# Optimization experiments

Hardware: AMD Instinct MI355X
Metric: run time of the kernel (lower is better)

## Reference

```python
import jax, jax.numpy as jnp
import numpy as np

E = 2048
H = 16
DH = E // H  # 128
B, T = 2, 2048
EPS = 1e-8


def rmsnorm(x, g):
    rms = jnp.sqrt(jnp.mean(x * x, axis=-1, keepdims=True) + EPS)
    return g * (x / rms)


def setup_inputs() -> dict:
    key = jax.random.key(0)
    ks = jax.random.split(key, 16)
    s_in = 1.0 / np.sqrt(E)
    s_ff = 1.0 / np.sqrt(4 * E)
    return {
        "x": jax.random.normal(ks[0], (B, T, E), dtype=jnp.float32),
        # stacked per-head QKV projections, stored (in, out) so y = x @ W + b
        "wq": jax.random.normal(ks[1], (H, E, DH), dtype=jnp.float32) * s_in,
        "bq": jax.random.normal(ks[2], (H, DH), dtype=jnp.float32) * s_in,
        "wk": jax.random.normal(ks[3], (H, E, DH), dtype=jnp.float32) * s_in,
        "bk": jax.random.normal(ks[4], (H, DH), dtype=jnp.float32) * s_in,
        "wv": jax.random.normal(ks[5], (H, E, DH), dtype=jnp.float32) * s_in,
        "bv": jax.random.normal(ks[6], (H, DH), dtype=jnp.float32) * s_in,
        "wo": jax.random.normal(ks[7], (E, E), dtype=jnp.float32) * s_in,
        "bo": jax.random.normal(ks[8], (E,), dtype=jnp.float32) * s_in,
        "w1": jax.random.normal(ks[9], (E, 4 * E), dtype=jnp.float32) * s_in,
        "b1": jax.random.normal(ks[10], (4 * E,), dtype=jnp.float32) * s_in,
        "w2": jax.random.normal(ks[11], (4 * E, E), dtype=jnp.float32) * s_ff,
        "b2": jax.random.normal(ks[12], (E,), dtype=jnp.float32) * s_ff,
        "g1": jnp.ones((E,), dtype=jnp.float32),
        "g2": jnp.ones((E,), dtype=jnp.float32),
    }


def reference(x, wq, bq, wk, bk, wv, bv, wo, bo, w1, b1, w2, b2, g1, g2):
    b, t, e = x.shape
    # --- attention sublayer ---
    h = rmsnorm(x, g1)
    q = jnp.einsum("bte,hed->bhtd", h, wq) + bq[None, :, None, :]
    k = jnp.einsum("bte,hed->bhtd", h, wk) + bk[None, :, None, :]
    v = jnp.einsum("bte,hed->bhtd", h, wv) + bv[None, :, None, :]
    scores = jnp.einsum("bhtd,bhsd->bhts", q, k) / jnp.sqrt(jnp.float32(DH))
    causal = jnp.tril(jnp.ones((t, t), dtype=bool))
    scores = jnp.where(causal[None, None], scores, -jnp.inf)
    w = jax.nn.softmax(scores, axis=-1)
    o = jnp.einsum("bhts,bhsd->bhtd", w, v)
    o = o.transpose(0, 2, 1, 3).reshape(b, t, e)  # concat heads on last dim
    x = x + o @ wo + bo
    # --- FFN sublayer (exact GELU, dropout is identity at inference) ---
    h = rmsnorm(x, g2)
    x = x + jax.nn.gelu(h @ w1 + b1, approximate=False) @ w2 + b2
    return x
```

## Files before the change

### kernel.cpp

```cpp
#include <hip/hip_runtime.h>
#include <hip/hip_bf16.h>

typedef unsigned short u16;
typedef unsigned int   u32;
typedef __attribute__((ext_vector_type(8))) short short8;
typedef __attribute__((ext_vector_type(4))) float f32x4;
typedef __attribute__((ext_vector_type(4))) unsigned short u16x4;

#define E_    2048
#define H_    16
#define DH_   128
#define B_    2
#define T_    2048
#define NTOK  4096
#define QKVN  6144

#define VMCNT(n) asm volatile("s_waitcnt vmcnt(" #n ")" ::: "memory")
#define LGKM0()  asm volatile("s_waitcnt lgkmcnt(0)" ::: "memory")

__device__ __forceinline__ u16 f2bf(float f) {
  union { float f; u32 u; } v; v.f = f;
  u32 r = (v.u + 0x7FFFu + ((v.u >> 16) & 1u)) >> 16;
  return (u16)r;
}

__global__ __launch_bounds__(256) void tr64(
    const float* __restrict__ in, u16* __restrict__ out,
    int R, int C, size_t inZ, size_t outZ)
{
  __shared__ float t[64][65];
  const float* ib = in + (size_t)blockIdx.z * inZ;
  u16* ob = out + (size_t)blockIdx.z * outZ;
  const int r0 = blockIdx.y * 64, c0 = blockIdx.x * 64;
  const int tid = threadIdx.x;
  const int rr = tid >> 4;
  const int cc = (tid & 15) * 4;
  #pragma unroll
  for (int p = 0; p < 4; ++p) {
    const float4 v = *(const float4*)(ib + (size_t)(r0 + p * 16 + rr) * C + c0 + cc);
    t[cc + 0][p * 16 + rr] = v.x;
    t[cc + 1][p * 16 + rr] = v.y;
    t[cc + 2][p * 16 + rr] = v.z;
    t[cc + 3][p * 16 + rr] = v.w;
  }
  __syncthreads();
  const int wr = tid >> 3;
  const int wc = (tid & 7) * 8;
  #pragma unroll
  for (int p = 0; p < 2; ++p) {
    short8 s;
    #pragma unroll
    for (int j = 0; j < 8; ++j) s[j] = (short)f2bf(t[p * 32 + wr][wc + j]);
    *(short8*)(ob + (size_t)(c0 + p * 32 + wr) * R + r0 + wc) = s;
  }
}

__global__ __launch_bounds__(256) void bias_cat(
    const float* __restrict__ bq, const float* __restrict__ bk,
    const float* __restrict__ bv, float* __restrict__ bias)
{
  int idx = blockIdx.x * 256 + threadIdx.x;
  const float* bb = (idx < 2048) ? bq : (idx < 4096) ? bk : bv;
  bias[idx] = bb[idx & 2047];
}

__global__ __launch_bounds__(256) void rmsnorm_k(
    const float* __restrict__ x, const float* __restrict__ g, u16* __restrict__ o)
{
  const int row = blockIdx.x;
  const float4* xr = (const float4*)(x + (size_t)row * E_);
  const float4* gr = (const float4*)g;
  const int tid = threadIdx.x;
  float4 a0 = xr[tid], a1 = xr[tid + 256];
  float s = a0.x*a0.x + a0.y*a0.y + a0.z*a0.z + a0.w*a0.w
          + a1.x*a1.x + a1.y*a1.y + a1.z*a1.z + a1.w*a1.w;
  #pragma unroll
  for (int m = 1; m < 64; m <<= 1) s += __shfl_xor(s, m);
  __shared__ float wsum[4];
  if ((tid & 63) == 0) wsum[tid >> 6] = s;
  __syncthreads();
  float tot = wsum[0] + wsum[1] + wsum[2] + wsum[3];
  float rinv = rsqrtf(tot * (1.0f / E_) + 1e-8f);
  float4 g0 = gr[tid], g1 = gr[tid + 256];
  u16x4 o0, o1;
  o0[0] = f2bf(a0.x * g0.x * rinv); o0[1] = f2bf(a0.y * g0.y * rinv);
  o0[2] = f2bf(a0.z * g0.z * rinv); o0[3] = f2bf(a0.w * g0.w * rinv);
  o1[0] = f2bf(a1.x * g1.x * rinv); o1[1] = f2bf(a1.y * g1.y * rinv);
  o1[2] = f2bf(a1.z * g1.z * rinv); o1[3] = f2bf(a1.w * g1.w * rinv);
  u16x4* orow = (u16x4*)(o + (size_t)row * E_);
  orow[tid] = o0;
  orow[tid + 256] = o1;
}

__device__ __forceinline__ void gload_lds16(const void* g, u16* lds_base) {
  __builtin_amdgcn_global_load_lds(
      (const __attribute__((address_space(1))) u32*)g,
      (__attribute__((address_space(3))) u32*)lds_base, 16, 0, 0);
}

template<int BM, int BN, int EPI>
__global__ __launch_bounds__(512, 2)
void gemm3(const u16* __restrict__ A, const u16* __restrict__ Bt,
           const float* __restrict__ bias, const float* __restrict__ resid,
           void* __restrict__ out, int M, int N, int K)
{
  constexpr int WROWS = BM / 2;
  constexpr int WCOLS = BN / 4;
  constexpr int MR    = WROWS / 16;
  constexpr int BUF   = (BM + BN) * 32;
  __shared__ __align__(16) u16 sh[3 * BUF];

  const int tid  = threadIdx.x;
  const int lane = tid & 63;
  const int l15  = lane & 15, lg = lane >> 4;
  const int w    = tid >> 6;
  const int wm   = w >> 2;
  const int wn   = w & 3;
  const int xs   = (l15 >> 1) & 3;

  const int nbx = N / BN;
  const int nwg = nbx * (M / BM);
  const int q8  = nwg >> 3;
  const int sid = (blockIdx.x & 7) * q8 + (blockIdx.x >> 3);
  const int m0  = (sid / nbx) * BM;
  const int n0  = (sid % nbx) * BN;

  const int r0 = tid >> 2;
  const int c0 = (((tid & 3) ^ ((tid >> 3) & 3)) * 8);
  const u16* gA  = A  + (size_t)(m0 + r0) * K + c0;
  const u16* gB  = Bt + (size_t)(n0 + r0) * K + c0;
  const u16* gA2 = gA + (size_t)128 * K;
  const u16* gB2 = gB + (size_t)128 * K;
  const int wub = (tid & ~63) * 8;

  f32x4 acc[MR][4] = {};
  const int NT = K >> 5;

  #pragma unroll
  for (int t = 0; t < 2; ++t) {
    u16* wb = sh + t * BUF;
    const int kS = t * 32;
    if constexpr (BM == 256) {
      gload_lds16(gA  + kS, wb + wub);
      gload_lds16(gA2 + kS, wb + 512 * 8 + wub);
      gload_lds16(gB  + kS, wb + 1024 * 8 + wub);
      gload_lds16(gB2 + kS, wb + 1536 * 8 + wub);
    } else {
      gload_lds16(gA  + kS, wb + wub);
      gload_lds16(gB  + kS, wb + 512 * 8 + wub);
      gload_lds16(gB2 + kS, wb + 1024 * 8 + wub);
    }
  }
  if constexpr (BM == 256) VMCNT(4); else VMCNT(3);
  __builtin_amdgcn_s_barrier();
  __builtin_amdgcn_sched_barrier(0);

  int b0 = 0, b2 = 2;
  #pragma unroll 1
  for (int i = 0; i < NT; ++i) {
    const u16* rb = sh + b0 * BUF;
    u16* wb = sh + b2 * BUF;
    const bool st = (i + 2 < NT);
    const int kS = (i + 2) << 5;
    short8 af[4], bf[4];

    if constexpr (BM == 256) {
      #pragma unroll
      for (int n = 0; n < 4; ++n)
        bf[n] = *(const short8*)(rb + BM * 32 + (wn * WCOLS + n * 16 + l15) * 32 + ((lg ^ xs) * 8));
      #pragma unroll
      for (int m = 0; m < 4; ++m)
        af[m] = *(const short8*)(rb + (wm * WROWS + m * 16 + l15) * 32 + ((lg ^ xs) * 8));
      if (st) {
        gload_lds16(gA + kS, wb + wub);
        gload_lds16(gB + kS, wb + 1024 * 8 + wub);
      }
      __builtin_amdgcn_s_barrier();
      LGKM0();
      __builtin_amdgcn_sched_barrier(0);
      __builtin_amdgcn_s_setprio(1);
      #pragma unroll
      for (int m = 0; m < 4; ++m)
        #pragma unroll
        for (int n = 0; n < 4; ++n)
          acc[m][n] = __builtin_amdgcn_mfma_f32_16x16x32_bf16(af[m], bf[n], acc[m][n], 0, 0, 0);
      __builtin_amdgcn_s_setprio(0);
      __builtin_amdgcn_s_barrier();
      __builtin_amdgcn_sched_barrier(0);
      #pragma unroll
      for (int m = 0; m < 4; ++m)
        af[m] = *(const short8*)(rb + (wm * WROWS + (4 + m) * 16 + l15) * 32 + ((lg ^ xs) * 8));
      if (st) {
        gload_lds16(gA2 + kS, wb + 512 * 8 + wub);
        gload_lds16(gB2 + kS, wb + 1536 * 8 + wub);
      }
      __builtin_amdgcn_s_barrier();
      LGKM0();
      __builtin_amdgcn_sched_barrier(0);
      __builtin_amdgcn_s_setprio(1);
      #pragma unroll
      for (int m = 0; m < 4; ++m)
        #pragma unroll
        for (int n = 0; n < 4; ++n)
          acc[4 + m][n] = __builtin_amdgcn_mfma_f32_16x16x32_bf16(af[m], bf[n], acc[4 + m][n], 0, 0, 0);
      __builtin_amdgcn_s_setprio(0);
      VMCNT(4);
      __builtin_amdgcn_s_barrier();
      __builtin_amdgcn_sched_barrier(0);
    } else {
      #pragma unroll
      for (int n = 0; n < 4; ++n)
        bf[n] = *(const short8*)(rb + BM * 32 + (wn * WCOLS + n * 16 + l15) * 32 + ((lg ^ xs) * 8));
      #pragma unroll
      for (int m = 0; m < 4; ++m)
        af[m] = *(const short8*)(rb + (wm * WROWS + m * 16 + l15) * 32 + ((lg ^ xs) * 8));
      if (st) {
        gload_lds16(gA  + kS, wb + wub);
        gload_lds16(gB  + kS, wb + 512 * 8 + wub);
        gload_lds16(gB2 + kS, wb + 1024 * 8 + wub);
      }
      __builtin_amdgcn_s_barrier();
      LGKM0();
      __builtin_amdgcn_sched_barrier(0);
      __builtin_amdgcn_s_setprio(1);
      #pragma unroll
      for (int m = 0; m < 4; ++m)
        #pragma unroll
        for (int n = 0; n < 4; ++n)
          acc[m][n] = __builtin_amdgcn_mfma_f32_16x16x32_bf16(af[m], bf[n], acc[m][n], 0, 0, 0);
      __builtin_amdgcn_s_setprio(0);
      VMCNT(3);
      __builtin_amdgcn_s_barrier();
      __builtin_amdgcn_sched_barrier(0);
    }
    b0 = (b0 == 2) ? 0 : b0 + 1;
    b2 = (b2 == 2) ? 0 : b2 + 1;
  }

  float bv[4];
  #pragma unroll
  for (int n = 0; n < 4; ++n) bv[n] = bias[n0 + wn * WCOLS + n * 16 + l15];

  if constexpr (EPI == 1) {
    #pragma unroll
    for (int n = 0; n < 4; ++n) {
      const int col = n0 + wn * WCOLS + n * 16 + l15;
      #pragma unroll
      for (int m = 0; m < MR; ++m)
        #pragma unroll
        for (int r = 0; r < 4; ++r) {
          const int row = m0 + wm * WROWS + m * 16 + lg * 4 + r;
          const size_t off = (size_t)row * N + col;
          ((float*)out)[off] = acc[m][n][r] + bv[n] + resid[off];
        }
    }
  } else {
    u16* ep = sh + w * 1024;
    #pragma unroll
    for (int m = 0; m < MR; ++m) {
      LGKM0();
      __builtin_amdgcn_sched_barrier(0);
      #pragma unroll
      for (int n = 0; n < 4; ++n)
        #pragma unroll
        for (int r = 0; r < 4; ++r) {
          float v = acc[m][n][r] + bv[n];
          if (EPI == 2) v = 0.5f * v * (1.0f + erff(v * 0.70710678118654752f));
          ep[(lg * 4 + r) * 64 + n * 16 + l15] = f2bf(v);
        }
      LGKM0();
      __builtin_amdgcn_sched_barrier(0);
      const int row0 = m0 + wm * WROWS + m * 16;
      #pragma unroll
      for (int it = 0; it < 2; ++it) {
        const int ch = it * 64 + lane;
        const int rr = ch >> 3, c8 = ch & 7;
        short8 s = *(const short8*)(ep + rr * 64 + c8 * 8);
        *(short8*)((u16*)out + (size_t)(row0 + rr) * N + n0 + wn * WCOLS + c8 * 8) = s;
      }
    }
  }
}

__global__ __launch_bounds__(256) void vtrans_k(
    const u16* __restrict__ qkv, u16* __restrict__ vt)
{
  __shared__ u16 tile[DH_][66];
  const int tid = threadIdx.x;
  const int bid = blockIdx.x;
  const int tt = bid & 31;
  const int bh = bid >> 5;
  const int b  = bh >> 4, h = bh & 15;
  const int t0 = tt * 64;
  const u16* src = qkv + (size_t)b * T_ * QKVN + 2 * E_ + h * DH_;
  #pragma unroll
  for (int it = 0; it < 8; ++it) {
    int c = it * 256 + tid;
    int t = c >> 5, dc = c & 31;
    u16x4 v = *(const u16x4*)(src + (size_t)(t0 + t) * QKVN + dc * 4);
    #pragma unroll
    for (int j = 0; j < 4; ++j) tile[dc * 4 + j][t] = v[j];
  }
  __syncthreads();
  u16* dst = vt + (size_t)bh * DH_ * T_ + t0;
  #pragma unroll
  for (int it = 0; it < 8; ++it) {
    int c = it * 256 + tid;
    int d = c >> 4, tc = c & 15;
    u16x4 v;
    #pragma unroll
    for (int j = 0; j < 4; ++j) v[j] = tile[d][tc * 4 + j];
    *(u16x4*)(dst + (size_t)d * T_ + tc * 4) = v;
  }
}

__global__ __launch_bounds__(256) void attn_k(
    const u16* __restrict__ qkv, const u16* __restrict__ vt, u16* __restrict__ o)
{
  const int tid  = threadIdx.x;
  const int lane = tid & 63;
  const int w    = tid >> 6;
  const int l15  = lane & 15, lg = lane >> 4;
  const int bid  = blockIdx.x;
  const int pair = bid & 31;
  const int qt   = 15 - (bid >> 5);
  const int h    = pair & 15;
  const int b    = pair >> 4;
  const int Q0 = qt * 128;
  const int qw = Q0 + w * 32;

  __shared__ __align__(16) u16 Ks[2][64 * 128];
  __shared__ __align__(16) u16 Vs[2][128 * 64];
  __shared__ __align__(16) u16 Ps[4][32 * 64];

  const u16* qb  = qkv + (size_t)b * T_ * QKVN + h * DH_;
  const u16* kb  = qb + E_;
  const u16* vtb = vt + (size_t)(b * H_ + h) * DH_ * T_;

  short8 qf[2][4];
  #pragma unroll
  for (int qi = 0; qi < 2; ++qi)
    #pragma unroll
    for (int kk = 0; kk < 4; ++kk)
      qf[qi][kk] = *(const short8*)(qb + (size_t)(qw + qi * 16 + l15) * QKVN + kk * 32 + lg * 8);

  f32x4 oacc[2][8] = {};
  float m_[2][4], l_[2][4];
  #pragma unroll
  for (int qi = 0; qi < 2; ++qi)
    #pragma unroll
    for (int r = 0; r < 4; ++r) { m_[qi][r] = -1e30f; l_[qi][r] = 0.f; }

  const int xr = l15 & 7;
  const float scl = 0.08838834764831845f;
  const int nt = Q0 / 64 + 2;
  const int qmaxw = qw + 31;
  const int wub = (tid & ~63);

  const u16* kp[4]; const u16* vp[4];
  #pragma unroll
  for (int i = 0; i < 4; ++i) {
    int f = i * 256 + tid;
    int r = f >> 4, p = f & 15, c = p ^ (r & 7);
    kp[i] = kb + (size_t)r * QKVN + c * 8;
  }
  #pragma unroll
  for (int i = 0; i < 4; ++i) {
    int f = i * 256 + tid;
    int d = f >> 3, p = f & 7, c = p ^ (d & 7);
    vp[i] = vtb + (size_t)d * T_ + c * 8;
  }

  auto STAGEKV = [&](int s0, int bufi) {
    const size_t ko = (size_t)s0 * QKVN;
    #pragma unroll
    for (int i = 0; i < 4; ++i)
      gload_lds16(kp[i] + ko, &Ks[bufi][(i * 256 + wub) * 8]);
    #pragma unroll
    for (int i = 0; i < 4; ++i)
      gload_lds16(vp[i] + s0, &Vs[bufi][(i * 256 + wub) * 8]);
  };

  STAGEKV(0, 0);
  VMCNT(0);
  __builtin_amdgcn_s_barrier();
  __builtin_amdgcn_sched_barrier(0);

  #pragma unroll 1
  for (int st = 0; st < nt; ++st) {
    const int s0 = st * 64;
    const int cur = st & 1;
    if (st + 1 < nt) STAGEKV(s0 + 64, cur ^ 1);

    if (s0 <= qmaxw) {
      const u16* Kc = Ks[cur];
      const u16* Vc = Vs[cur];
      f32x4 sc[2][4] = {};
      __builtin_amdgcn_s_setprio(1);
      #pragma unroll
      for (int sj = 0; sj < 4; ++sj) {
        const int row = sj * 16 + l15;
        #pragma unroll
        for (int kk = 0; kk < 4; ++kk) {
          short8 kfr = *(const short8*)(Kc + row * 128 + (((kk * 4 + lg) ^ xr) * 8));
          sc[0][sj] = __builtin_amdgcn_mfma_f32_16x16x32_bf16(qf[0][kk], kfr, sc[0][sj], 0, 0, 0);
          sc[1][sj] = __builtin_amdgcn_mfma_f32_16x16x32_bf16(qf[1][kk], kfr, sc[1][sj], 0, 0, 0);
        }
      }
      __builtin_amdgcn_s_setprio(0);
      const bool needmask = (s0 + 63 > qw);
      #pragma unroll
      for (int qi = 0; qi < 2; ++qi)
        #pragma unroll
        for (int sj = 0; sj < 4; ++sj)
          #pragma unroll
          for (int r = 0; r < 4; ++r) {
            float v = sc[qi][sj][r] * scl;
            if (needmask) {
              int s = s0 + sj * 16 + l15;
              int q = qw + qi * 16 + lg * 4 + r;
              if (s > q) v = -1e30f;
            }
            sc[qi][sj][r] = v;
          }
      #pragma unroll
      for (int qi = 0; qi < 2; ++qi) {
        float tmax[4], alpha[4], rsum[4];
        #pragma unroll
        for (int r = 0; r < 4; ++r)
          tmax[r] = fmaxf(fmaxf(sc[qi][0][r], sc[qi][1][r]), fmaxf(sc[qi][2][r], sc[qi][3][r]));
        #pragma unroll
        for (int r = 0; r < 4; ++r)
          #pragma unroll
          for (int m = 1; m < 16; m <<= 1) tmax[r] = fmaxf(tmax[r], __shfl_xor(tmax[r], m));
        #pragma unroll
        for (int r = 0; r < 4; ++r) {
          float mn = fmaxf(m_[qi][r], tmax[r]);
          alpha[r] = __expf(m_[qi][r] - mn);
          m_[qi][r] = mn;
          rsum[r] = 0.f;
        }
        #pragma unroll
        for (int sj = 0; sj < 4; ++sj)
          #pragma unroll
          for (int r = 0; r < 4; ++r) {
            float p = __expf(sc[qi][sj][r] - m_[qi][r]);
            rsum[r] += p;
            const int row = qi * 16 + lg * 4 + r;
            const int ch  = (sj * 2 + (l15 >> 3)) ^ (row & 7);
            Ps[w][row * 64 + ch * 8 + (l15 & 7)] = f2bf(p);
          }
        #pragma unroll
        for (int r = 0; r < 4; ++r) {
          #pragma unroll
          for (int m = 1; m < 16; m <<= 1) rsum[r] += __shfl_xor(rsum[r], m);
          l_[qi][r] = l_[qi][r] * alpha[r] + rsum[r];
        }
        #pragma unroll
        for (int dj = 0; dj < 8; ++dj)
          #pragma unroll
          for (int r = 0; r < 4; ++r) oacc[qi][dj][r] *= alpha[r];
      }
      LGKM0();
      __builtin_amdgcn_sched_barrier(0);
      __builtin_amdgcn_s_setprio(1);
      #pragma unroll
      for (int ks = 0; ks < 2; ++ks) {
        short8 pf0 = *(const short8*)(&Ps[w][l15 * 64 + (((ks * 4 + lg) ^ xr) * 8)]);
        short8 pf1 = *(const short8*)(&Ps[w][(16 + l15) * 64 + (((ks * 4 + lg) ^ xr) * 8)]);
        #pragma unroll
        for (int dj = 0; dj < 8; ++dj) {
          const int row = dj * 16 + l15;
          short8 vfr = *(const short8*)(Vc + row * 64 + (((ks * 4 + lg) ^ xr) * 8));
          oacc[0][dj] = __builtin_amdgcn_mfma_f32_16x16x32_bf16(pf0, vfr, oacc[0][dj], 0, 0, 0);
          oacc[1][dj] = __builtin_amdgcn_mfma_f32_16x16x32_bf16(pf1, vfr, oacc[1][dj], 0, 0, 0);
        }
      }
      __builtin_amdgcn_s_setprio(0);
    }
    VMCNT(0);
    __builtin_amdgcn_s_barrier();
    __builtin_amdgcn_sched_barrier(0);
  }

  float inv[2][4];
  #pragma unroll
  for (int qi = 0; qi < 2; ++qi)
    #pragma unroll
    for (int r = 0; r < 4; ++r) inv[qi][r] = 1.0f / l_[qi][r];
  u16* ob = o + (size_t)(b * T_ + qw) * E_ + h * DH_;
  #pragma unroll
  for (int qi = 0; qi < 2; ++qi)
    #pragma unroll
    for (int dj = 0; dj < 8; ++dj)
      #pragma unroll
      for (int r = 0; r < 4; ++r)
        ob[(size_t)(qi * 16 + lg * 4 + r) * E_ + dj * 16 + l15] = f2bf(oacc[qi][dj][r] * inv[qi][r]);
}

extern "C" void kernel_launch(void* const* d_in, const int* in_sizes, int n_in,
                              void* d_out, int out_size, void* d_ws, size_t ws_size,
                              hipStream_t stream)
{
  const float* x  = (const float*)d_in[0];
  const float* wq = (const float*)d_in[1];
  const float* bq = (const float*)d_in[2];
  const float* wk = (const float*)d_in[3];
  const float* bk = (const float*)d_in[4];
  const float* wv = (const float*)d_in[5];
  const float* bv = (const float*)d_in[6];
  const float* wo = (const float*)d_in[7];
  const float* bo = (const float*)d_in[8];
  const float* w1 = (const float*)d_in[9];
  const float* b1 = (const float*)d_in[10];
  const float* w2 = (const float*)d_in[11];
  const float* b2 = (const float*)d_in[12];
  const float* g1 = (const float*)d_in[13];
  const float* g2 = (const float*)d_in[14];
  float* xout = (float*)d_out;

  if (ws_size < 201351168u) return;

  char* ws = (char*)d_ws;
  u16*   wqkv_t = (u16*)(ws + 0);
  u16*   h1     = (u16*)(ws + 25165824);
  u16*   qkv    = (u16*)(ws + 41943040);
  u16*   vt     = (u16*)(ws + 92274688);
  u16*   o_     = (u16*)(ws + 109051904);
  u16*   wo_t   = (u16*)(ws + 125829120);
  u16*   w1_t   = (u16*)(ws + 134217728);
  u16*   w2_t   = (u16*)(ws + 167772160);
  float* bqkv   = (float*)(ws + 201326592);
  u16*   u_     = (u16*)(ws + 0);
  u16*   h2     = vt;
  float* x2     = xout;

  tr64<<<dim3(2, 32, 16), 256, 0, stream>>>(wq, wqkv_t,                          E_, DH_, (size_t)E_ * DH_, (size_t)DH_ * E_);
  tr64<<<dim3(2, 32, 16), 256, 0, stream>>>(wk, wqkv_t + (size_t)E_ * E_,        E_, DH_, (size_t)E_ * DH_, (size_t)DH_ * E_);
  tr64<<<dim3(2, 32, 16), 256, 0, stream>>>(wv, wqkv_t + (size_t)2 * E_ * E_,    E_, DH_, (size_t)E_ * DH_, (size_t)DH_ * E_);
  tr64<<<dim3(32, 32, 1),  256, 0, stream>>>(wo, wo_t, E_, E_, 0, 0);
  tr64<<<dim3(128, 32, 1), 256, 0, stream>>>(w1, w1_t, E_, 4 * E_, 0, 0);
  tr64<<<dim3(32, 128, 1), 256, 0, stream>>>(w2, w2_t, 4 * E_, E_, 0, 0);
  bias_cat<<<24, 256, 0, stream>>>(bq, bk, bv, bqkv);

  rmsnorm_k<<<NTOK, 256, 0, stream>>>(x, g1, h1);
  gemm3<128, 256, 0><<<(NTOK / 128) * (QKVN / 256), 512, 0, stream>>>(h1, wqkv_t, bqkv, nullptr, qkv, NTOK, QKVN, E_);
  vtrans_k<<<B_ * H_ * (T_ / 64), 256, 0, stream>>>(qkv, vt);
  attn_k<<<B_ * H_ * (T_ / 16 / 8), 256, 0, stream>>>(qkv, vt, o_);
  gemm3<128, 256, 1><<<(NTOK / 128) * (E_ / 256), 512, 0, stream>>>(o_, wo_t, bo, x, x2, NTOK, E_, E_);
  rmsnorm_k<<<NTOK, 256, 0, stream>>>(x2, g2, h2);
  gemm3<256, 256, 2><<<(NTOK / 256) * (4 * E_ / 256), 512, 0, stream>>>(h2, w1_t, b1, nullptr, u_, NTOK, 4 * E_, E_);
  gemm3<128, 256, 1><<<(NTOK / 128) * (E_ / 256), 512, 0, stream>>>(u_, w2_t, b2, x2, xout, NTOK, E_, 4 * E_);
}
```

Baseline: 728.3 us.

## Unroll GEMM K-loop by three buffers and drop manual lgkm waits and sched barriers

The GEMM main loop is unrolled three ways through a macro, so the triple-buffer indices become compile-time constants instead of rotating runtime variables. The tail drains vmcnt to zero on the last tiles. Explicit lgkmcnt(0) waits and sched_barrier fences are removed from the GEMM and attention loops, which lets the compiler interleave LDS reads with MFMAs. This gives up the hand-enforced instruction ordering, and it depends on the compiler inserting correct waits for LDS reads that are consumed after s_barrier, which is a correctness risk.

```diff
diff --git a/kernel.cpp b/kernel.cpp
--- a/kernel.cpp
+++ b/kernel.cpp
@@ -16,7 +16,6 @@
 #define QKVN  6144
 
 #define VMCNT(n) asm volatile("s_waitcnt vmcnt(" #n ")" ::: "memory")
-#define LGKM0()  asm volatile("s_waitcnt lgkmcnt(0)" ::: "memory")
 
 __device__ __forceinline__ u16 f2bf(float f) {
   union { float f; u32 u; } v; v.f = f;
@@ -153,89 +152,90 @@
   }
   if constexpr (BM == 256) VMCNT(4); else VMCNT(3);
   __builtin_amdgcn_s_barrier();
-  __builtin_amdgcn_sched_barrier(0);
-
-  int b0 = 0, b2 = 2;
+
+  int i = 0;
+
+#define KTILE(CUR, STG)                                                          \
+  do {                                                                           \
+    const u16* rb = sh + (CUR) * BUF;                                            \
+    u16* wb = sh + (STG) * BUF;                                                  \
+    const bool st = (i + 2 < NT);                                                \
+    const int kS = (i + 2) << 5;                                                 \
+    const int rem = NT - 1 - i;                                                  \
+    short8 af[4], bf[4];                                                         \
+    if constexpr (BM == 256) {                                                   \
+      _Pragma("unroll")                                                          \
+      for (int n = 0; n < 4; ++n)                                                \
+        bf[n] = *(const short8*)(rb + BM * 32 + (wn * WCOLS + n * 16 + l15) * 32 + ((lg ^ xs) * 8)); \
+      _Pragma("unroll")                                                          \
+      for (int m = 0; m < 4; ++m)                                                \
+        af[m] = *(const short8*)(rb + (wm * WROWS + m * 16 + l15) * 32 + ((lg ^ xs) * 8)); \
+      if (st) {                                                                  \
+        gload_lds16(gA + kS, wb + wub);                                          \
+        gload_lds16(gB + kS, wb + 1024 * 8 + wub);                               \
+      }                                                                          \
+      __builtin_amdgcn_s_barrier();                                              \
+      __builtin_amdgcn_s_setprio(1);                                             \
+      _Pragma("unroll")                                                          \
+      for (int m = 0; m < 4; ++m)                                                \
+        _Pragma("unroll")                                                        \
+        for (int n = 0; n < 4; ++n)                                              \
+          acc[m][n] = __builtin_amdgcn_mfma_f32_16x16x32_bf16(af[m], bf[n], acc[m][n], 0, 0, 0); \
+      __builtin_amdgcn_s_setprio(0);                                             \
+      __builtin_amdgcn_s_barrier();                                              \
+      _Pragma("unroll")                                                          \
+      for (int m = 0; m < 4; ++m)                                                \
+        af[m] = *(const short8*)(rb + (wm * WROWS + (4 + m) * 16 + l15) * 32 + ((lg ^ xs) * 8)); \
+      if (st) {                                                                  \
+        gload_lds16(gA2 + kS, wb + 512 * 8 + wub);                               \
+        gload_lds16(gB2 + kS, wb + 1536 * 8 + wub);                              \
+      }                                                                          \
+      __builtin_amdgcn_s_barrier();                                              \
+      __builtin_amdgcn_s_setprio(1);                                             \
+      _Pragma("unroll")                                                          \
+      for (int m = 0; m < 4; ++m)                                                \
+        _Pragma("unroll")                                                        \
+        for (int n = 0; n < 4; ++n)                                              \
+          acc[4 + m][n] = __builtin_amdgcn_mfma_f32_16x16x32_bf16(af[m], bf[n], acc[4 + m][n], 0, 0, 0); \
+      __builtin_amdgcn_s_setprio(0);                                             \
+      if (rem >= 2) { VMCNT(4); } else { VMCNT(0); }                             \
+      __builtin_amdgcn_s_barrier();                                              \
+    } else {                                                                     \
+      _Pragma("unroll")                                                          \
+      for (int n = 0; n < 4; ++n)                                                \
+        bf[n] = *(const short8*)(rb + BM * 32 + (wn * WCOLS + n * 16 + l15) * 32 + ((lg ^ xs) * 8)); \
+      _Pragma("unroll")                                                          \
+      for (int m = 0; m < 4; ++m)                                                \
+        af[m] = *(const short8*)(rb + (wm * WROWS + m * 16 + l15) * 32 + ((lg ^ xs) * 8)); \
+      if (st) {                                                                  \
+        gload_lds16(gA  + kS, wb + wub);                                         \
+        gload_lds16(gB  + kS, wb + 512 * 8 + wub);                               \
+        gload_lds16(gB2 + kS, wb + 1024 * 8 + wub);                              \
+      }                                                                          \
+      __builtin_amdgcn_s_barrier();                                              \
+      __builtin_amdgcn_s_setprio(1);                                             \
+      _Pragma("unroll")                                                          \
+      for (int m = 0; m < 4; ++m)                                                \
+        _Pragma("unroll")                                                        \
+        for (int n = 0; n < 4; ++n)                                              \
+          acc[m][n] = __builtin_amdgcn_mfma_f32_16x16x32_bf16(af[m], bf[n], acc[m][n], 0, 0, 0); \
+      __builtin_amdgcn_s_setprio(0);                                             \
+      if (rem >= 2) { VMCNT(3); } else { VMCNT(0); }                             \
+      __builtin_amdgcn_s_barrier();                                              \
+    }                                                                            \
+    ++i;                                                                         \
+  } while (0)
+
+  const int trips = NT / 3;
   #pragma unroll 1
-  for (int i = 0; i < NT; ++i) {
-    const u16* rb = sh + b0 * BUF;
-    u16* wb = sh + b2 * BUF;
-    const bool st = (i + 2 < NT);
-    const int kS = (i + 2) << 5;
-    short8 af[4], bf[4];
-
-    if constexpr (BM == 256) {
-      #pragma unroll
-      for (int n = 0; n < 4; ++n)
-        bf[n] = *(const short8*)(rb + BM * 32 + (wn * WCOLS + n * 16 + l15) * 32 + ((lg ^ xs) * 8));
-      #pragma unroll
-      for (int m = 0; m < 4; ++m)
-        af[m] = *(const short8*)(rb + (wm * WROWS + m * 16 + l15) * 32 + ((lg ^ xs) * 8));
-      if (st) {
-        gload_lds16(gA + kS, wb + wub);
-        gload_lds16(gB + kS, wb + 1024 * 8 + wub);
-      }
-      __builtin_amdgcn_s_barrier();
-      LGKM0();
-      __builtin_amdgcn_sched_barrier(0);
-      __builtin_amdgcn_s_setprio(1);
-      #pragma unroll
-      for (int m = 0; m < 4; ++m)
-        #pragma unroll
-        for (int n = 0; n < 4; ++n)
-          acc[m][n] = __builtin_amdgcn_mfma_f32_16x16x32_bf16(af[m], bf[n], acc[m][n], 0, 0, 0);
-      __builtin_amdgcn_s_setprio(0);
-      __builtin_amdgcn_s_barrier();
-      __builtin_amdgcn_sched_barrier(0);
-      #pragma unroll
-      for (int m = 0; m < 4; ++m)
-        af[m] = *(const short8*)(rb + (wm * WROWS + (4 + m) * 16 + l15) * 32 + ((lg ^ xs) * 8));
-      if (st) {
-        gload_lds16(gA2 + kS, wb + 512 * 8 + wub);
-        gload_lds16(gB2 + kS, wb + 1536 * 8 + wub);
-      }
-      __builtin_amdgcn_s_barrier();
-      LGKM0();
-      __builtin_amdgcn_sched_barrier(0);
-      __builtin_amdgcn_s_setprio(1);
-      #pragma unroll
-      for (int m = 0; m < 4; ++m)
-        #pragma unroll
-        for (int n = 0; n < 4; ++n)
-          acc[4 + m][n] = __builtin_amdgcn_mfma_f32_16x16x32_bf16(af[m], bf[n], acc[4 + m][n], 0, 0, 0);
-      __builtin_amdgcn_s_setprio(0);
-      VMCNT(4);
-      __builtin_amdgcn_s_barrier();
-      __builtin_amdgcn_sched_barrier(0);
-    } else {
-      #pragma unroll
-      for (int n = 0; n < 4; ++n)
-        bf[n] = *(const short8*)(rb + BM * 32 + (wn * WCOLS + n * 16 + l15) * 32 + ((lg ^ xs) * 8));
-      #pragma unroll
-      for (int m = 0; m < 4; ++m)
-        af[m] = *(const short8*)(rb + (wm * WROWS + m * 16 + l15) * 32 + ((lg ^ xs) * 8));
-      if (st) {
-        gload_lds16(gA  + kS, wb + wub);
-        gload_lds16(gB  + kS, wb + 512 * 8 + wub);
-        gload_lds16(gB2 + kS, wb + 1024 * 8 + wub);
-      }
-      __builtin_amdgcn_s_barrier();
-      LGKM0();
-      __builtin_amdgcn_sched_barrier(0);
-      __builtin_amdgcn_s_setprio(1);
-      #pragma unroll
-      for (int m = 0; m < 4; ++m)
-        #pragma unroll
-        for (int n = 0; n < 4; ++n)
-          acc[m][n] = __builtin_amdgcn_mfma_f32_16x16x32_bf16(af[m], bf[n], acc[m][n], 0, 0, 0);
-      __builtin_amdgcn_s_setprio(0);
-      VMCNT(3);
-      __builtin_amdgcn_s_barrier();
-      __builtin_amdgcn_sched_barrier(0);
-    }
-    b0 = (b0 == 2) ? 0 : b0 + 1;
-    b2 = (b2 == 2) ? 0 : b2 + 1;
-  }
+  for (int t = 0; t < trips; ++t) {
+    KTILE(0, 2);
+    KTILE(1, 0);
+    KTILE(2, 1);
+  }
+  if (i < NT) KTILE(0, 2);
+  if (i < NT) KTILE(1, 0);
+#undef KTILE
 
   float bv[4];
   #pragma unroll
@@ -258,8 +258,6 @@
     u16* ep = sh + w * 1024;
     #pragma unroll
     for (int m = 0; m < MR; ++m) {
-      LGKM0();
-      __builtin_amdgcn_sched_barrier(0);
       #pragma unroll
       for (int n = 0; n < 4; ++n)
         #pragma unroll
@@ -268,8 +266,7 @@
           if (EPI == 2) v = 0.5f * v * (1.0f + erff(v * 0.70710678118654752f));
           ep[(lg * 4 + r) * 64 + n * 16 + l15] = f2bf(v);
         }
-      LGKM0();
-      __builtin_amdgcn_sched_barrier(0);
+      asm volatile("s_waitcnt lgkmcnt(0)" ::: "memory");
       const int row0 = m0 + wm * WROWS + m * 16;
       #pragma unroll
       for (int it = 0; it < 2; ++it) {
@@ -278,6 +275,7 @@
         short8 s = *(const short8*)(ep + rr * 64 + c8 * 8);
         *(short8*)((u16*)out + (size_t)(row0 + rr) * N + n0 + wn * WCOLS + c8 * 8) = s;
       }
+      asm volatile("s_waitcnt lgkmcnt(0)" ::: "memory");
     }
   }
 }
@@ -384,7 +382,6 @@
   STAGEKV(0, 0);
   VMCNT(0);
   __builtin_amdgcn_s_barrier();
-  __builtin_amdgcn_sched_barrier(0);
 
   #pragma unroll 1
   for (int st = 0; st < nt; ++st) {
@@ -461,8 +458,6 @@
           #pragma unroll
           for (int r = 0; r < 4; ++r) oacc[qi][dj][r] *= alpha[r];
       }
-      LGKM0();
-      __builtin_amdgcn_sched_barrier(0);
       __builtin_amdgcn_s_setprio(1);
       #pragma unroll
       for (int ks = 0; ks < 2; ++ks) {
@@ -480,7 +475,6 @@
     }
     VMCNT(0);
     __builtin_amdgcn_s_barrier();
-    __builtin_amdgcn_sched_barrier(0);
   }
 
   float inv[2][4];
```

Measured after the change: 711.3 us. 1.02x faster.
